# Kernel tuning notes

Hardware: AMD Instinct MI355X
Metric: run time of the kernel (lower is better)

The kernel has to match this reference:

```python
import jax, jax.numpy as jnp
import numpy as np


def lstm_cell(x, h, c, Wih, Whh, bih, bhh):
    # PyTorch LSTM gate order: i, f, g, o
    gates = x @ Wih.T + h @ Whh.T + bih + bhh
    i, f, g, o = jnp.split(gates, 4, axis=-1)
    c_new = jax.nn.sigmoid(f) * c + jax.nn.sigmoid(i) * jnp.tanh(g)
    h_new = jax.nn.sigmoid(o) * jnp.tanh(c_new)
    return h_new, c_new


def setup_inputs() -> dict:
    V, E, H, L, S, B, T = 100000, 256, 256, 2, 256, 16, 128
    G = 4 * H
    s = 0.1  # weight scale to keep activations/gradients well-conditioned
    key = jax.random.key(0)
    ks = jax.random.split(key, 16)
    return {
        'source': jax.random.randint(ks[0], (S, B), 0, V),
        'target_size': T,
        'target_embeddings': jax.random.normal(ks[1], (T, 1, E), dtype=jnp.float32),
        'h0': jax.random.normal(ks[2], (L, B, H), dtype=jnp.float32) * s,
        'c0': jax.random.normal(ks[3], (L, B, H), dtype=jnp.float32) * s,
        'embed_table': jax.random.normal(ks[4], (V, E), dtype=jnp.float32) * s,
        'enc_Wih': jax.random.normal(ks[5], (L, G, E), dtype=jnp.float32) * s,
        'enc_Whh': jax.random.normal(ks[6], (L, G, H), dtype=jnp.float32) * s,
        'enc_bih': jax.random.normal(ks[7], (L, G), dtype=jnp.float32) * s,
        'enc_bhh': jax.random.normal(ks[8], (L, G), dtype=jnp.float32) * s,
        'dec_Wih': jax.random.normal(ks[9], (L, G, E), dtype=jnp.float32) * s,
        'dec_Whh': jax.random.normal(ks[10], (L, G, H), dtype=jnp.float32) * s,
        'dec_bih': jax.random.normal(ks[11], (L, G), dtype=jnp.float32) * s,
        'dec_bhh': jax.random.normal(ks[12], (L, G), dtype=jnp.float32) * s,
        'attn_W': jax.random.normal(ks[13], (1, 2 * H), dtype=jnp.float32) * s,
        'attn_b': jnp.zeros((1,), dtype=jnp.float32),
        'comb_W': jax.random.normal(ks[14], (H, 2 * H), dtype=jnp.float32) * s,
        'comb_b': jnp.zeros((H,), dtype=jnp.float32),
    }


def reference(source, target_size, target_embeddings, h0, c0, embed_table,
              enc_Wih, enc_Whh, enc_bih, enc_bhh,
              dec_Wih, dec_Whh, dec_bih, dec_bhh,
              attn_W, attn_b, comb_W, comb_b):
    L = h0.shape[0]
    B = source.shape[1]

    # ---------------- encoder (per-step LSTM loop -> layer-wise scans) ----
    x = embed_table[source]  # [S, B, E]  (dropout is identity at eval)
    h_fin = []
    for l in range(L):
        def step(carry, xt, l=l):
            h, c = carry
            h, c = lstm_cell(xt, h, c, enc_Wih[l], enc_Whh[l], enc_bih[l], enc_bhh[l])
            return (h, c), h
        (hL, cL), x = jax.lax.scan(step, (h0[l], c0[l]), x)
        h_fin.append(hL)
    hidden_final = jnp.stack(h_fin)   # [L, B, H] == hiddens[-1] in the source
    enc_outputs = x                   # [S, B, H] last-layer hidden per step
    S = enc_outputs.shape[0]

    # NOTE (faithful to source bugs): seq2seq sets both decoder hidden AND
    # cell from encoder_hidden[-1], and the decoder runs its LSTM on the raw
    # input `embedding`, discarding the attention-combined output.
    x0 = jnp.tile(target_embeddings[0, 0], (B, 1))  # [B, E]

    def dec_step(carry, _):
        x, h, c = carry
        # per-step Bahdanau-style attention: computed but UNUSED, as in source
        cat = jnp.concatenate([jnp.broadcast_to(x, (S,) + x.shape), enc_outputs], axis=-1)
        w = jax.nn.softmax(cat @ attn_W.T + attn_b, axis=0)       # [S, B, 1]
        applied = (w * enc_outputs).sum(0)                         # [B, H]
        _combined = jax.nn.relu(jnp.concatenate([x, applied], axis=-1) @ comb_W.T + comb_b)
        # actual recurrence: multi-layer LSTM on the raw input x
        inp = x
        hs, cs = [], []
        for l in range(h.shape[0]):
            hl, cl = lstm_cell(inp, h[l], c[l], dec_Wih[l], dec_Whh[l], dec_bih[l], dec_bhh[l])
            hs.append(hl)
            cs.append(cl)
            inp = hl
        return (inp, jnp.stack(hs), jnp.stack(cs)), inp

    _, ys = jax.lax.scan(dec_step, (x0, hidden_final, hidden_final), None,
                         length=target_size - 1)  # ys: [T-1, B, H]
    H = ys.shape[-1]
    preds = jnp.zeros((target_size, 1, B, H), ys.dtype)
    preds = preds.at[1:].set(ys[:, None])  # predictions[0] stays zero
    return preds
```

## Files before the change

kernel.cpp:

```cpp
#include <hip/hip_runtime.h>
#include <hip/hip_bf16.h>

typedef __attribute__((ext_vector_type(8))) short short8;
typedef __attribute__((ext_vector_type(4))) float f32x4;

#define SEQ   256
#define BB    16
#define EE    256
#define HH    256
#define GG    1024
#define TT    128
#define NWG   32
#define KP    264
#define SLOT_S 8192
#define SENT  0xFF80FF80u
#define MAXTRY (1 << 20)

__device__ __forceinline__ float sigm(float x) { return 1.0f / (1.0f + __expf(-x)); }
__device__ __forceinline__ float tanh_f(float x) {
    float e = __expf(2.0f * x);
    return 1.0f - 2.0f / (e + 1.0f);
}
__device__ __forceinline__ void split2s(float v, short* hi, short* lo) {
    __hip_bfloat16 h = __float2bfloat16(v);
    __hip_bfloat16 l = __float2bfloat16(v - __bfloat162float(h));
    *hi = *(short*)&h; *lo = *(short*)&l;
}
__device__ __forceinline__ f32x4 MFMA(short8 a, short8 b, f32x4 c) {
    return __builtin_amdgcn_mfma_f32_16x16x32_bf16(a, b, c, 0, 0, 0);
}

__device__ __forceinline__ short8 ld16s(const short* p) {
    short8 r;
    asm volatile("global_load_dwordx4 %0, %1, off sc0 sc1" : "=v"(r) : "v"(p));
    return r;
}
__device__ __forceinline__ void st4s(int* p, int v) {
    asm volatile("global_store_dword %0, %1, off sc0 sc1" :: "v"(p), "v"(v) : "memory");
}
__device__ __forceinline__ void vmwait() {
    asm volatile("s_waitcnt vmcnt(0)" ::: "memory");
    __builtin_amdgcn_sched_barrier(0);
}
union U8 { short8 s; unsigned u[4]; };
__device__ __forceinline__ unsigned chk(short8 f) {
    U8 x; x.s = f;
    return (unsigned)((x.u[0] == SENT) | (x.u[1] == SENT) | (x.u[2] == SENT) | (x.u[3] == SENT));
}

__global__ void k_sent(unsigned* p) {
    long i = ((long)blockIdx.x * 256 + threadIdx.x) * 4;
    p[i] = SENT; p[i + 1] = SENT; p[i + 2] = SENT; p[i + 3] = SENT;
}

__global__ void k_cvt2(const float* __restrict__ s, __hip_bfloat16* __restrict__ hi,
                       __hip_bfloat16* __restrict__ lo, int n) {
    int i = blockIdx.x * 256 + threadIdx.x;
    if (i < n) {
        short a, b; split2s(s[i], &a, &b);
        hi[i] = *(__hip_bfloat16*)&a; lo[i] = *(__hip_bfloat16*)&b;
    }
}

__global__ void k_zero(float* __restrict__ p) {
    p[blockIdx.x * 256 + threadIdx.x] = 0.0f;
}

__global__ void k_embed(const int* __restrict__ src, const float* __restrict__ tab,
                        __hip_bfloat16* __restrict__ xhi, __hip_bfloat16* __restrict__ xlo) {
    int r = blockIdx.x;
    int j = threadIdx.x;
    long idx = src[r];
    short a, b; split2s(tab[idx * EE + j], &a, &b);
    xhi[(long)r * EE + j] = *(__hip_bfloat16*)&a;
    xlo[(long)r * EE + j] = *(__hip_bfloat16*)&b;
}

__global__ void __launch_bounds__(256) k_gemm_in(
        const __hip_bfloat16* __restrict__ Xhi, const __hip_bfloat16* __restrict__ Xlo,
        const __hip_bfloat16* __restrict__ Whi, const __hip_bfloat16* __restrict__ Wlo,
        const float* __restrict__ bih, const float* __restrict__ bhh,
        float* __restrict__ gates) {
    int lane = threadIdx.x & 63, w = threadIdx.x >> 6;
    int m0 = (blockIdx.x >> 4) * 16;
    int n0 = ((blockIdx.x & 15) * 4 + w) * 16;
    int cc = lane & 15, g = lane >> 4;
    int koff = g * 8;
    const short* xh = (const short*)Xhi + (long)(m0 + cc) * EE + koff;
    const short* xl = (const short*)Xlo + (long)(m0 + cc) * EE + koff;
    const short* wh = (const short*)Whi + (long)(n0 + cc) * EE + koff;
    const short* wl = (const short*)Wlo + (long)(n0 + cc) * EE + koff;
    f32x4 acc1 = {0.f, 0.f, 0.f, 0.f}, acc2 = {0.f, 0.f, 0.f, 0.f};
#pragma unroll
    for (int k = 0; k < EE; k += 32) {
        short8 ah = *(const short8*)(xh + k), al = *(const short8*)(xl + k);
        short8 bh = *(const short8*)(wh + k), bl = *(const short8*)(wl + k);
        acc1 = MFMA(ah, bh, acc1);
        acc2 = MFMA(ah, bl, acc2);
        acc2 = MFMA(al, bh, acc2);
    }
    f32x4 acc = acc1 + acc2;
    int ncol = n0 + cc;
    float bias = bih[ncol] + bhh[ncol];
    int mrow = m0 + g * 4;
#pragma unroll
    for (int r = 0; r < 4; ++r)
        gates[(long)(mrow + r) * GG + ncol] = acc[r] + bias;
}

__device__ __forceinline__ void load_wslice(const short* __restrict__ Wg, int j0,
                                            short* __restrict__ Wl) {
    int tid = threadIdx.x;
    int lr = tid >> 3;
    int q = lr >> 3, jl = lr & 7;
    const short* src = Wg + (long)(q * 256 + j0 + jl) * 256;
    short* dst = Wl + lr * KP;
#pragma unroll
    for (int s = 0; s < 4; ++s) {
        int c = (tid & 7) * 8 + s * 64;
        *(short8*)(dst + c) = *(const short8*)(src + c);
    }
}


__global__ void __launch_bounds__(256, 1) k_enc_coop(
        const float* __restrict__ gates0,
        const short* __restrict__ Whh0h, const short* __restrict__ Whh0l,
        const short* __restrict__ Wih1h, const short* __restrict__ Wih1l,
        const short* __restrict__ Whh1h, const short* __restrict__ Whh1l,
        const float* __restrict__ bih1, const float* __restrict__ bhh1,
        const float* __restrict__ h0p, const float* __restrict__ c0p,
        short* __restrict__ H0, short* __restrict__ H1,
        float* __restrict__ hfin) {
    __shared__ short Wl[6][32 * KP];
    __shared__ float gacc[2][8][16][17];

    int tid = threadIdx.x, bid = blockIdx.x;
    int j0 = bid * 8;
    load_wslice(Whh0h, j0, Wl[0]); load_wslice(Whh0l, j0, Wl[1]);
    load_wslice(Wih1h, j0, Wl[2]); load_wslice(Wih1l, j0, Wl[3]);
    load_wslice(Whh1h, j0, Wl[4]); load_wslice(Whh1l, j0, Wl[5]);

    int bb = (tid & 127) >> 3, jl = tid & 7, j = j0 + jl, lay = tid >> 7;
    float creg = c0p[lay * 4096 + bb * 256 + j];
    float bs[4] = {0.f, 0.f, 0.f, 0.f};
    if (lay) {
#pragma unroll
        for (int q = 0; q < 4; ++q) bs[q] = bih1[q * 256 + j] + bhh1[q * 256 + j];
    }
    {
        float hv = h0p[lay * 4096 + bb * 256 + j];
        short sh, sl; split2s(hv, &sh, &sl);
        int mh = (unsigned short)sh, ml = (unsigned short)sl;
        int nh = __shfl_down(mh, 1), nl = __shfl_down(ml, 1);
        int* dst = (int*)(lay ? H1 : H0);
        if (!(jl & 1)) {
            int idx = bb * 256 + bid * 8 + (jl >> 1);
            st4s(dst + idx, mh | (nh << 16));
            st4s(dst + idx + 4, ml | (nl << 16));
        }
    }

    int lane = tid & 63, w = tid >> 6, cc = lane & 15, g4 = lane >> 4, koff = g4 * 8;
    int tw = w & 1, kb = (w >> 1) * 128;
    int abase = cc * 512 + kb * 2 + g4 * 16;
    int wr = (tw * 16 + cc) * KP + kb + koff;

    for (int i = 0; i <= SEQ; ++i) {
        bool actL0 = (i < SEQ), actL1 = (i >= 1);
        int par = i & 1;

        float gpre[4];
        if (!lay && actL0) {
#pragma unroll
            for (int q = 0; q < 4; ++q)
                gpre[q] = gates0[(long)(i * BB + bb) * GG + q * 256 + j];
        }

        short8 f0h[4], f0l[4], f1h[4], f1l[4];
        const short* b0 = H0 + (long)i * SLOT_S + abase;
        const short* b1 = H1 + (long)(i - 1) * SLOT_S + abase;
        int tries = 0;
        while (true) {
#pragma unroll
            for (int ki = 0; ki < 4; ++ki) {
                f0h[ki] = ld16s(b0 + ki * 64);
                f0l[ki] = ld16s(b0 + ki * 64 + 8);
            }
            if (actL1) {
#pragma unroll
                for (int ki = 0; ki < 4; ++ki) {
                    f1h[ki] = ld16s(b1 + ki * 64);
                    f1l[ki] = ld16s(b1 + ki * 64 + 8);
                }
            }
            vmwait();
            unsigned bad = 0;
#pragma unroll
            for (int ki = 0; ki < 4; ++ki) bad |= chk(f0h[ki]) | chk(f0l[ki]);
            if (actL1) {
#pragma unroll
                for (int ki = 0; ki < 4; ++ki) bad |= chk(f1h[ki]) | chk(f1l[ki]);
            }
            if (!__any((int)bad) || ++tries > MAXTRY) break;
        }

        f32x4 z = {0.f, 0.f, 0.f, 0.f};
        f32x4 s0 = z, s1 = z;
        if (actL0) {
            f32x4 a1 = z, a2 = z;
#pragma unroll
            for (int ki = 0; ki < 4; ++ki) {
                short8 wh  = *(const short8*)(Wl[0] + wr + ki * 32);
                short8 wl2 = *(const short8*)(Wl[1] + wr + ki * 32);
                a1 = MFMA(f0h[ki], wh, a1);
                a2 = MFMA(f0h[ki], wl2, a2);
                a2 = MFMA(f0l[ki], wh, a2);
            }
            s0 = a1 + a2;
        }
        if (actL1) {
            f32x4 a1 = z, a2 = z;
#pragma unroll
            for (int ki = 0; ki < 4; ++ki) {
                a1 = MFMA(f0h[ki], *(const short8*)(Wl[2] + wr + ki * 32), a1);
                a2 = MFMA(f0h[ki], *(const short8*)(Wl[3] + wr + ki * 32), a2);
                a2 = MFMA(f0l[ki], *(const short8*)(Wl[2] + wr + ki * 32), a2);
                a1 = MFMA(f1h[ki], *(const short8*)(Wl[4] + wr + ki * 32), a1);
                a2 = MFMA(f1h[ki], *(const short8*)(Wl[5] + wr + ki * 32), a2);
                a2 = MFMA(f1l[ki], *(const short8*)(Wl[4] + wr + ki * 32), a2);
            }
            s1 = a1 + a2;
        }
#pragma unroll
        for (int r = 0; r < 4; ++r) {
            gacc[par][w][g4 * 4 + r][cc] = s0[r];
            gacc[par][4 + w][g4 * 4 + r][cc] = s1[r];
        }
        __syncthreads();

        bool act = lay ? actL1 : actL0;
        if (act) {
            int t = lay ? (i - 1) : i;
            float gv[4];
#pragma unroll
            for (int q = 0; q < 4; ++q) {
                int lr = q * 8 + jl, tl = lr >> 4, c = lr & 15;
                gv[q] = lay ? (gacc[par][4 + tl][bb][c] + gacc[par][6 + tl][bb][c] + bs[q])
                            : (gacc[par][tl][bb][c] + gacc[par][2 + tl][bb][c] + gpre[q]);
            }
            float c = sigm(gv[1]) * creg + sigm(gv[0]) * tanh_f(gv[2]);
            creg = c;
            float h = sigm(gv[3]) * tanh_f(c);
            short sh, sl; split2s(h, &sh, &sl);
            int mh = (unsigned short)sh, ml = (unsigned short)sl;
            int nh = __shfl_down(mh, 1), nl = __shfl_down(ml, 1);
            int* dst = (int*)(lay ? (H1 + (long)i * SLOT_S) : (H0 + (long)(i + 1) * SLOT_S));
            if (!(jl & 1)) {
                int idx = bb * 256 + bid * 8 + (jl >> 1);
                st4s(dst + idx, mh | (nh << 16));
                st4s(dst + idx + 4, ml | (nl << 16));
            }
            if (t == SEQ - 1) hfin[lay * 4096 + bb * 256 + j] = h;
        }
    }
}

__global__ void __launch_bounds__(256, 1) k_dec_coop(
        const short* __restrict__ Wihh, const short* __restrict__ Wihl,
        const short* __restrict__ Whhh, const short* __restrict__ Whhl,
        const float* __restrict__ dbih, const float* __restrict__ dbhh,
        const float* __restrict__ tef, const float* __restrict__ hfin,
        short* __restrict__ H0, short* __restrict__ H1,
        short* __restrict__ TE,
        float* __restrict__ preds) {
    __shared__ short Wl[8][32 * KP];
    __shared__ float gacc[2][4][16][17];
    const int WN = GG * EE;

    int tid = threadIdx.x, bid = blockIdx.x;
    int j0 = bid * 8;
    load_wslice(Wihh, j0, Wl[0]);      load_wslice(Wihl, j0, Wl[1]);
    load_wslice(Whhh, j0, Wl[2]);      load_wslice(Whhl, j0, Wl[3]);
    load_wslice(Wihh + WN, j0, Wl[4]); load_wslice(Wihl + WN, j0, Wl[5]);
    load_wslice(Whhh + WN, j0, Wl[6]); load_wslice(Whhl + WN, j0, Wl[7]);

    int bb = (tid & 127) >> 3, jl = tid & 7, j = j0 + jl;
    float c0r = 0.f, c1r = 0.f;
    float bs0[4] = {0,0,0,0}, bs1[4] = {0,0,0,0};
    if (tid < 128) {
        float h0v = hfin[bb * 256 + j], h1v = hfin[4096 + bb * 256 + j];
        c0r = h0v; c1r = h1v;
        int idx = bb * 256 + bid * 8 + (jl >> 1);
        short sh, sl;
        split2s(tef[j], &sh, &sl);
        {
            int mh = (unsigned short)sh, ml = (unsigned short)sl;
            int nh = __shfl_down(mh, 1), nl = __shfl_down(ml, 1);
            if (!(jl & 1)) { st4s((int*)TE + idx, mh | (nh << 16));
                             st4s((int*)TE + idx + 4, ml | (nl << 16)); }
        }
        split2s(h0v, &sh, &sl);
        {
            int mh = (unsigned short)sh, ml = (unsigned short)sl;
            int nh = __shfl_down(mh, 1), nl = __shfl_down(ml, 1);
            if (!(jl & 1)) { st4s((int*)H0 + idx, mh | (nh << 16));
                             st4s((int*)H0 + idx + 4, ml | (nl << 16)); }
        }
        split2s(h1v, &sh, &sl);
        {
            int mh = (unsigned short)sh, ml = (unsigned short)sl;
            int nh = __shfl_down(mh, 1), nl = __shfl_down(ml, 1);
            if (!(jl & 1)) { st4s((int*)H1 + idx, mh | (nh << 16));
                             st4s((int*)H1 + idx + 4, ml | (nl << 16)); }
        }
#pragma unroll
        for (int q = 0; q < 4; ++q) {
            bs0[q] = dbih[q*256+j] + dbhh[q*256+j];
            bs1[q] = dbih[GG + q*256+j] + dbhh[GG + q*256+j];
        }
    }

    int lane = tid & 63, w = tid >> 6, cc = lane & 15, g4 = lane >> 4, koff = g4 * 8;
    int tw = w & 1, kb = (w >> 1) * 128;
    int abase = cc * 512 + kb * 2 + g4 * 16;
    int wr = (tw * 16 + cc) * KP + kb + koff;

    short8 xAh[4], xAl[4], xBh[4], xBl[4], h1ih[4], h1il[4];

    {
        const short* p0 = H0 + abase;
        const short* p1 = H1 + abase;
        int tries = 0;
        while (true) {
#pragma unroll
            for (int ki = 0; ki < 4; ++ki) {
                xBh[ki] = ld16s(p0 + ki * 64); xBl[ki] = ld16s(p0 + ki * 64 + 8);
                h1ih[ki] = ld16s(p1 + ki * 64); h1il[ki] = ld16s(p1 + ki * 64 + 8);
            }
            vmwait();
            unsigned bad = 0;
#pragma unroll
            for (int ki = 0; ki < 4; ++ki)
                bad |= chk(xBh[ki]) | chk(xBl[ki]) | chk(h1ih[ki]) | chk(h1il[ki]);
            if (!__any((int)bad) || ++tries > MAXTRY) break;
        }
    }

    for (int t = 0; t < TT - 1; ++t) {
        {
            const short* px = (t ? H1 + (long)t * SLOT_S : TE) + abase;
            int tries = 0;
            while (true) {
#pragma unroll
                for (int ki = 0; ki < 4; ++ki) {
                    xAh[ki] = ld16s(px + ki * 64); xAl[ki] = ld16s(px + ki * 64 + 8);
                }
                vmwait();
                unsigned bad = 0;
#pragma unroll
                for (int ki = 0; ki < 4; ++ki) bad |= chk(xAh[ki]) | chk(xAl[ki]);
                if (!__any((int)bad) || ++tries > MAXTRY) break;
            }
            f32x4 a1 = {0.f,0.f,0.f,0.f}, a2 = {0.f,0.f,0.f,0.f};
#pragma unroll
            for (int ki = 0; ki < 4; ++ki) {
                a1 = MFMA(xAh[ki], *(const short8*)(Wl[0] + wr + ki * 32), a1);
                a2 = MFMA(xAh[ki], *(const short8*)(Wl[1] + wr + ki * 32), a2);
                a2 = MFMA(xAl[ki], *(const short8*)(Wl[0] + wr + ki * 32), a2);
                a1 = MFMA(xBh[ki], *(const short8*)(Wl[2] + wr + ki * 32), a1);
                a2 = MFMA(xBh[ki], *(const short8*)(Wl[3] + wr + ki * 32), a2);
                a2 = MFMA(xBl[ki], *(const short8*)(Wl[2] + wr + ki * 32), a2);
            }
            f32x4 accs = a1 + a2;
#pragma unroll
            for (int r = 0; r < 4; ++r) gacc[0][w][g4 * 4 + r][cc] = accs[r];
        }
        __syncthreads();
        if (tid < 128) {
            float gv[4];
#pragma unroll
            for (int q = 0; q < 4; ++q) {
                int lr = q * 8 + jl;
                gv[q] = gacc[0][lr >> 4][bb][lr & 15] + gacc[0][2 + (lr >> 4)][bb][lr & 15] + bs0[q];
            }
            float c = sigm(gv[1]) * c0r + sigm(gv[0]) * tanh_f(gv[2]);
            c0r = c;
            float h = sigm(gv[3]) * tanh_f(c);
            short sh, sl; split2s(h, &sh, &sl);
            int mh = (unsigned short)sh, ml = (unsigned short)sl;
            int nh = __shfl_down(mh, 1), nl = __shfl_down(ml, 1);
            if (!(jl & 1)) {
                int idx = bb * 256 + bid * 8 + (jl >> 1);
                int* dst = (int*)(H0 + (long)(t + 1) * SLOT_S);
                st4s(dst + idx, mh | (nh << 16));
                st4s(dst + idx + 4, ml | (nl << 16));
            }
        }
        {
            const short* px = H0 + (long)(t + 1) * SLOT_S + abase;
            int tries = 0;
            while (true) {
#pragma unroll
                for (int ki = 0; ki < 4; ++ki) {
                    xBh[ki] = ld16s(px + ki * 64); xBl[ki] = ld16s(px + ki * 64 + 8);
                }
                vmwait();
                unsigned bad = 0;
#pragma unroll
                for (int ki = 0; ki < 4; ++ki) bad |= chk(xBh[ki]) | chk(xBl[ki]);
                if (!__any((int)bad) || ++tries > MAXTRY) break;
            }
            f32x4 a1 = {0.f,0.f,0.f,0.f}, a2 = {0.f,0.f,0.f,0.f};
#pragma unroll
            for (int ki = 0; ki < 4; ++ki) {
                short8 hh = t ? xAh[ki] : h1ih[ki];
                short8 hl = t ? xAl[ki] : h1il[ki];
                a1 = MFMA(xBh[ki], *(const short8*)(Wl[4] + wr + ki * 32), a1);
                a2 = MFMA(xBh[ki], *(const short8*)(Wl[5] + wr + ki * 32), a2);
                a2 = MFMA(xBl[ki], *(const short8*)(Wl[4] + wr + ki * 32), a2);
                a1 = MFMA(hh, *(const short8*)(Wl[6] + wr + ki * 32), a1);
                a2 = MFMA(hh, *(const short8*)(Wl[7] + wr + ki * 32), a2);
                a2 = MFMA(hl, *(const short8*)(Wl[6] + wr + ki * 32), a2);
            }
            f32x4 accs = a1 + a2;
#pragma unroll
            for (int r = 0; r < 4; ++r) gacc[1][w][g4 * 4 + r][cc] = accs[r];
        }
        __syncthreads();
        if (tid < 128) {
            float gv[4];
#pragma unroll
            for (int q = 0; q < 4; ++q) {
                int lr = q * 8 + jl;
                gv[q] = gacc[1][lr >> 4][bb][lr & 15] + gacc[1][2 + (lr >> 4)][bb][lr & 15] + bs1[q];
            }
            float c = sigm(gv[1]) * c1r + sigm(gv[0]) * tanh_f(gv[2]);
            c1r = c;
            float h = sigm(gv[3]) * tanh_f(c);
            short sh, sl; split2s(h, &sh, &sl);
            int mh = (unsigned short)sh, ml = (unsigned short)sl;
            int nh = __shfl_down(mh, 1), nl = __shfl_down(ml, 1);
            if (!(jl & 1)) {
                int idx = bb * 256 + bid * 8 + (jl >> 1);
                int* dst = (int*)(H1 + (long)(t + 1) * SLOT_S);
                st4s(dst + idx, mh | (nh << 16));
                st4s(dst + idx + 4, ml | (nl << 16));
            }
            preds[((long)(t + 1) * BB + bb) * HH + j] = h;
        }
    }
}

extern "C" void kernel_launch(void* const* d_in, const int* in_sizes, int n_in,
                              void* d_out, int out_size, void* d_ws, size_t ws_size,
                              hipStream_t stream) {
    const int*   src   = (const int*)  d_in[0];
    const float* te    = (const float*)d_in[2];
    const float* h0    = (const float*)d_in[3];
    const float* c0    = (const float*)d_in[4];
    const float* table = (const float*)d_in[5];
    const float* eWih  = (const float*)d_in[6];
    const float* eWhh  = (const float*)d_in[7];
    const float* ebih  = (const float*)d_in[8];
    const float* ebhh  = (const float*)d_in[9];
    const float* dWih  = (const float*)d_in[10];
    const float* dWhh  = (const float*)d_in[11];
    const float* dbih  = (const float*)d_in[12];
    const float* dbhh  = (const float*)d_in[13];
    float* preds = (float*)d_out;

    const int WN = GG * EE;
    const size_t MB = 1u << 20;
    char* ws = (char*)d_ws;
    short* eWih_hi = (short*)(ws + 0 * MB);
    short* eWih_lo = (short*)(ws + 1 * MB);
    short* eWhh_hi = (short*)(ws + 2 * MB);
    short* eWhh_lo = (short*)(ws + 3 * MB);
    short* dWih_hi = (short*)(ws + 4 * MB);
    short* dWih_lo = (short*)(ws + 5 * MB);
    short* dWhh_hi = (short*)(ws + 6 * MB);
    short* dWhh_lo = (short*)(ws + 7 * MB);
    short* Xa_hi   = (short*)(ws + 8 * MB);
    short* Xa_lo   = (short*)(ws + 10 * MB);
    float* hfin    = (float*)(ws + 12 * MB);
    short* slots   = (short*)(ws + 13 * MB);
    short* SLe0 = slots;
    short* SLe1 = SLe0 + (long)257 * SLOT_S;
    short* SLd0 = SLe1 + (long)257 * SLOT_S;
    short* SLd1 = SLd0 + (long)128 * SLOT_S;
    short* SLte = SLd1 + (long)128 * SLOT_S;
    float* gates0 = (float*)(ws + 26 * MB);

    const int NSLOT = 257 + 257 + 128 + 128 + 1;
    k_sent<<<3084, 256, 0, stream>>>((unsigned*)slots);

    k_cvt2<<<2048, 256, 0, stream>>>(eWih, (__hip_bfloat16*)eWih_hi, (__hip_bfloat16*)eWih_lo, 2 * WN);
    k_cvt2<<<2048, 256, 0, stream>>>(eWhh, (__hip_bfloat16*)eWhh_hi, (__hip_bfloat16*)eWhh_lo, 2 * WN);
    k_cvt2<<<2048, 256, 0, stream>>>(dWih, (__hip_bfloat16*)dWih_hi, (__hip_bfloat16*)dWih_lo, 2 * WN);
    k_cvt2<<<2048, 256, 0, stream>>>(dWhh, (__hip_bfloat16*)dWhh_hi, (__hip_bfloat16*)dWhh_lo, 2 * WN);

    k_embed<<<4096, 256, 0, stream>>>(src, table, (__hip_bfloat16*)Xa_hi, (__hip_bfloat16*)Xa_lo);
    k_gemm_in<<<4096, 256, 0, stream>>>((__hip_bfloat16*)Xa_hi, (__hip_bfloat16*)Xa_lo,
                                        (__hip_bfloat16*)eWih_hi, (__hip_bfloat16*)eWih_lo,
                                        ebih, ebhh, gates0);
    k_enc_coop<<<NWG, 256, 0, stream>>>(gates0, eWhh_hi, eWhh_lo,
                                        eWih_hi + WN, eWih_lo + WN, eWhh_hi + WN, eWhh_lo + WN,
                                        ebih + GG, ebhh + GG, h0, c0,
                                        SLe0, SLe1, hfin);

    k_dec_coop<<<NWG, 256, 0, stream>>>(dWih_hi, dWih_lo, dWhh_hi, dWhh_lo,
                                        dbih, dbhh, te, hfin,
                                        SLd0, SLd1, SLte, preds);

    k_zero<<<16, 256, 0, stream>>>(preds);
    (void)NSLOT; (void)in_sizes; (void)n_in; (void)out_size; (void)ws_size;
}
```

Baseline: 2.310 ms.

## Interleave gate layout, prefetch gates after spin-wait, fuse convert and zero launches

The input-gate GEMM now writes gates in a j-major interleaved layout so each encoder thread fetches its four gate preactivations with one 16-byte load. That load is issued one step ahead, after the spin-wait, so its latency overlaps the recurrence. The four weight-conversion launches are merged into one kernel, and zeroing the first prediction row moves into the decoder kernel, which removes two launches. The gates0 layout change must stay consistent between producer and consumer, and the whole thing still depends on how the serial recurrence dominates.

```diff
diff --git a/kernel.cpp b/kernel.cpp
--- a/kernel.cpp
+++ b/kernel.cpp
@@ -53,17 +53,16 @@
     p[i] = SENT; p[i + 1] = SENT; p[i + 2] = SENT; p[i + 3] = SENT;
 }
 
-__global__ void k_cvt2(const float* __restrict__ s, __hip_bfloat16* __restrict__ hi,
-                       __hip_bfloat16* __restrict__ lo, int n) {
-    int i = blockIdx.x * 256 + threadIdx.x;
-    if (i < n) {
-        short a, b; split2s(s[i], &a, &b);
-        hi[i] = *(__hip_bfloat16*)&a; lo[i] = *(__hip_bfloat16*)&b;
-    }
-}
-
-__global__ void k_zero(float* __restrict__ p) {
-    p[blockIdx.x * 256 + threadIdx.x] = 0.0f;
+__global__ void k_cvt4(const float* __restrict__ s0, const float* __restrict__ s1,
+                       const float* __restrict__ s2, const float* __restrict__ s3,
+                       char* __restrict__ ws) {
+    int g = blockIdx.x >> 11;
+    int i = (blockIdx.x & 2047) * 256 + threadIdx.x;
+    const float* s = (g == 0) ? s0 : (g == 1) ? s1 : (g == 2) ? s2 : s3;
+    __hip_bfloat16* hi = (__hip_bfloat16*)(ws + ((size_t)2 * g) * (1u << 20));
+    __hip_bfloat16* lo = (__hip_bfloat16*)(ws + ((size_t)2 * g + 1) * (1u << 20));
+    short a, b; split2s(s[i], &a, &b);
+    hi[i] = *(__hip_bfloat16*)&a; lo[i] = *(__hip_bfloat16*)&b;
 }
 
 __global__ void k_embed(const int* __restrict__ src, const float* __restrict__ tab,
@@ -102,10 +101,11 @@
     f32x4 acc = acc1 + acc2;
     int ncol = n0 + cc;
     float bias = bih[ncol] + bhh[ncol];
+    int jj = ncol & 255, qq = ncol >> 8;
     int mrow = m0 + g * 4;
 #pragma unroll
     for (int r = 0; r < 4; ++r)
-        gates[(long)(mrow + r) * GG + ncol] = acc[r] + bias;
+        gates[(long)(mrow + r) * GG + jj * 4 + qq] = acc[r] + bias;
 }
 
 __device__ __forceinline__ void load_wslice(const short* __restrict__ Wg, int j0,
@@ -148,6 +148,10 @@
 #pragma unroll
         for (int q = 0; q < 4; ++q) bs[q] = bih1[q * 256 + j] + bhh1[q * 256 + j];
     }
+    f32x4 gnew = {0.f, 0.f, 0.f, 0.f};
+    if (!lay) {
+        gnew = *(const f32x4*)(gates0 + ((long)bb * 256 + j) * 4);
+    }
     {
         float hv = h0p[lay * 4096 + bb * 256 + j];
         short sh, sl; split2s(hv, &sh, &sl);
@@ -161,21 +165,14 @@
         }
     }
 
-    int lane = tid & 63, w = tid >> 6, cc = lane & 15, g4 = lane >> 4, koff = g4 * 8;
+    int lane = tid & 63, w = tid >> 6, cc = lane & 15, g4 = lane >> 4;
     int tw = w & 1, kb = (w >> 1) * 128;
     int abase = cc * 512 + kb * 2 + g4 * 16;
-    int wr = (tw * 16 + cc) * KP + kb + koff;
+    int wr = (tw * 16 + cc) * KP + kb + (g4 * 8);
 
     for (int i = 0; i <= SEQ; ++i) {
         bool actL0 = (i < SEQ), actL1 = (i >= 1);
         int par = i & 1;
-
-        float gpre[4];
-        if (!lay && actL0) {
-#pragma unroll
-            for (int q = 0; q < 4; ++q)
-                gpre[q] = gates0[(long)(i * BB + bb) * GG + q * 256 + j];
-        }
 
         short8 f0h[4], f0l[4], f1h[4], f1l[4];
         const short* b0 = H0 + (long)i * SLOT_S + abase;
@@ -203,6 +200,14 @@
                 for (int ki = 0; ki < 4; ++ki) bad |= chk(f1h[ki]) | chk(f1l[ki]);
             }
             if (!__any((int)bad) || ++tries > MAXTRY) break;
+        }
+
+        float gpre[4] = {0.f, 0.f, 0.f, 0.f};
+        if (!lay) {
+#pragma unroll
+            for (int q = 0; q < 4; ++q) gpre[q] = gnew[q];
+            if (i + 1 < SEQ)
+                gnew = *(const f32x4*)(gates0 + ((long)((i + 1) * BB + bb) * 256 + j) * 4);
         }
 
         f32x4 z = {0.f, 0.f, 0.f, 0.f};
@@ -291,6 +296,7 @@
     if (tid < 128) {
         float h0v = hfin[bb * 256 + j], h1v = hfin[4096 + bb * 256 + j];
         c0r = h0v; c1r = h1v;
+        preds[bb * 256 + j] = 0.0f;
         int idx = bb * 256 + bid * 8 + (jl >> 1);
         short sh, sl;
         split2s(tef[j], &sh, &sl);
@@ -321,10 +327,10 @@
         }
     }
 
-    int lane = tid & 63, w = tid >> 6, cc = lane & 15, g4 = lane >> 4, koff = g4 * 8;
+    int lane = tid & 63, w = tid >> 6, cc = lane & 15, g4 = lane >> 4;
     int tw = w & 1, kb = (w >> 1) * 128;
     int abase = cc * 512 + kb * 2 + g4 * 16;
-    int wr = (tw * 16 + cc) * KP + kb + koff;
+    int wr = (tw * 16 + cc) * KP + kb + (g4 * 8);
 
     short8 xAh[4], xAl[4], xBh[4], xBl[4], h1ih[4], h1il[4];
 
@@ -492,13 +498,9 @@
     short* SLte = SLd1 + (long)128 * SLOT_S;
     float* gates0 = (float*)(ws + 26 * MB);
 
-    const int NSLOT = 257 + 257 + 128 + 128 + 1;
     k_sent<<<3084, 256, 0, stream>>>((unsigned*)slots);
 
-    k_cvt2<<<2048, 256, 0, stream>>>(eWih, (__hip_bfloat16*)eWih_hi, (__hip_bfloat16*)eWih_lo, 2 * WN);
-    k_cvt2<<<2048, 256, 0, stream>>>(eWhh, (__hip_bfloat16*)eWhh_hi, (__hip_bfloat16*)eWhh_lo, 2 * WN);
-    k_cvt2<<<2048, 256, 0, stream>>>(dWih, (__hip_bfloat16*)dWih_hi, (__hip_bfloat16*)dWih_lo, 2 * WN);
-    k_cvt2<<<2048, 256, 0, stream>>>(dWhh, (__hip_bfloat16*)dWhh_hi, (__hip_bfloat16*)dWhh_lo, 2 * WN);
+    k_cvt4<<<8192, 256, 0, stream>>>(eWih, eWhh, dWih, dWhh, ws);
 
     k_embed<<<4096, 256, 0, stream>>>(src, table, (__hip_bfloat16*)Xa_hi, (__hip_bfloat16*)Xa_lo);
     k_gemm_in<<<4096, 256, 0, stream>>>((__hip_bfloat16*)Xa_hi, (__hip_bfloat16*)Xa_lo,
@@ -512,7 +514,5 @@
     k_dec_coop<<<NWG, 256, 0, stream>>>(dWih_hi, dWih_lo, dWhh_hi, dWhh_lo,
                                         dbih, dbhh, te, hfin,
                                         SLd0, SLd1, SLte, preds);
-
-    k_zero<<<16, 256, 0, stream>>>(preds);
-    (void)NSLOT; (void)in_sizes; (void)n_in; (void)out_size; (void)ws_size;
-}
+    (void)in_sizes; (void)n_in; (void)out_size; (void)ws_size;
+}
```

Result: slower. 2.379 ms (+3.0%).
